# Kernel optimization log

Hardware: AMD Instinct MI355X
Metric: run time of the kernel (lower is better)

## Reference

```python
import jax, jax.numpy as jnp
import numpy as np

N_NODES = 16000
N_EDGES = 128000
IN_FEAT = 1024   # nb_iprs
OUT_FEAT = 1024  # RelGraphConv out / embed_dim
N_RELS = 7
NB_GOS = 4096


def setup_inputs() -> dict:
    key = jax.random.key(0)
    ks = jax.random.split(key, 9)
    feat = jax.random.normal(ks[0], (N_NODES, IN_FEAT), dtype=jnp.float32)
    src = jax.random.randint(ks[1], (N_EDGES,), 0, N_NODES, dtype=jnp.int32)
    dst = jax.random.randint(ks[2], (N_EDGES,), 0, N_NODES, dtype=jnp.int32)
    etypes = jax.random.randint(ks[3], (N_EDGES,), 0, N_RELS, dtype=jnp.int32)
    # RelGraphConv params (regularizer=None): per-relation weight, self-loop weight, bias
    s = 1.0 / np.sqrt(IN_FEAT)
    W_rel = jax.random.uniform(ks[4], (N_RELS, IN_FEAT, OUT_FEAT), dtype=jnp.float32, minval=-s, maxval=s)
    W_loop = jax.random.uniform(ks[5], (IN_FEAT, OUT_FEAT), dtype=jnp.float32, minval=-s, maxval=s)
    bias = jnp.zeros((OUT_FEAT,), dtype=jnp.float32)
    # GO embeddings, init U(-k, k) with k = sqrt(1/embed_dim)
    k = 1.0 / np.sqrt(OUT_FEAT)
    go_embed = jax.random.uniform(ks[6], (NB_GOS, OUT_FEAT), dtype=jnp.float32, minval=-k, maxval=k)
    go_rad = jax.random.uniform(ks[7], (NB_GOS, 1), dtype=jnp.float32, minval=-k, maxval=k)
    return {"feat": feat, "src": src, "dst": dst, "etypes": etypes,
            "W_rel": W_rel, "W_loop": W_loop, "bias": bias,
            "go_embed": go_embed, "go_rad": go_rad}


def reference(feat, src, dst, etypes, W_rel, W_loop, bias, go_embed, go_rad):
    n = feat.shape[0]
    # RelGraphConv (sum aggregation, self-loop, bias, no activation):
    # message on edge e: feat[src[e]] @ W_rel[etypes[e]]; by linearity, first
    # segment-sum source features per (dst, rel), then one batched GEMM.
    x_src = feat[src]                                   # [E, in]
    seg = dst.astype(jnp.int32) * N_RELS + etypes       # combined (dst, rel) id
    agg = jax.ops.segment_sum(x_src, seg, num_segments=n * N_RELS)
    agg = agg.reshape(n, N_RELS, IN_FEAT)               # [N, R, in]
    h = jnp.einsum('nri,rio->no', agg, W_rel) + feat @ W_loop + bias  # [N, out]
    # scoring: sigmoid(x @ E_go^T + |rad|)
    logits = jax.nn.sigmoid(h @ go_embed.T + jnp.abs(go_rad).reshape(1, -1))
    return logits
```

## Files before the change

kernel.cpp:

```cpp
#include <hip/hip_runtime.h>
#include <math.h>

#define N_NODES 16000
#define N_EDGES 128000
#define KDIM 1024
#define N_RELS 7
#define NB_GOS 4096
#define KCAT (KDIM * (N_RELS + 1))
#define MPAD 16128

#define BM 128
#define BN 128
#define BK 32
#define CAP2 (N_EDGES + N_RELS * BM)
#define NTILE_E (CAP2 / BM)

typedef __attribute__((ext_vector_type(8))) short bf16x8;
typedef __attribute__((ext_vector_type(8))) unsigned short u16x8;
typedef __attribute__((ext_vector_type(4))) float f32x4;

__device__ __forceinline__ unsigned short f2bf(float f) {
    union { float f; unsigned int u; } v; v.f = f;
    unsigned int u = v.u + 0x7FFFu + ((v.u >> 16) & 1u);
    return (unsigned short)(u >> 16);
}

__device__ __forceinline__ float bf2f(unsigned short u) {
    union { unsigned int u; float f; } v; v.u = (unsigned int)u << 16;
    return v.f;
}

__device__ __forceinline__ void gload16(const void* g, void* lds) {
    __builtin_amdgcn_global_load_lds(
        (const __attribute__((address_space(1))) unsigned int*)g,
        (__attribute__((address_space(3))) unsigned int*)lds, 16, 0, 0);
}


__global__ __launch_bounds__(256) void conv_bf16(const float* __restrict__ in,
                                                 unsigned short* __restrict__ out, int n8) {
    int i = blockIdx.x * 256 + threadIdx.x;
    if (i >= n8) return;
    const float4* in4 = (const float4*)in;
    float4 x = in4[2 * i], y = in4[2 * i + 1];
    u16x8 o;
    o[0] = f2bf(x.x); o[1] = f2bf(x.y); o[2] = f2bf(x.z); o[3] = f2bf(x.w);
    o[4] = f2bf(y.x); o[5] = f2bf(y.y); o[6] = f2bf(y.z); o[7] = f2bf(y.w);
    *(u16x8*)&out[(size_t)i * 8] = o;
}

__global__ __launch_bounds__(256) void conv_cat(const float* __restrict__ in,
                                                unsigned short* __restrict__ Acat) {
    int i = blockIdx.x * 256 + threadIdx.x;
    if (i >= N_NODES * (KDIM / 8)) return;
    int n = i >> 7, c8 = (i & 127) * 8;
    const float4* in4 = (const float4*)(in + (size_t)n * KDIM + c8);
    float4 x = in4[0], y = in4[1];
    u16x8 o;
    o[0] = f2bf(x.x); o[1] = f2bf(x.y); o[2] = f2bf(x.z); o[3] = f2bf(x.w);
    o[4] = f2bf(y.x); o[5] = f2bf(y.y); o[6] = f2bf(y.z); o[7] = f2bf(y.w);
    *(u16x8*)&Acat[(size_t)n * KCAT + c8] = o;
}

__global__ void transpose_w(const float* __restrict__ Wrel,
                            const float* __restrict__ Wloop,
                            unsigned short* __restrict__ WrelT,
                            unsigned short* __restrict__ WloopT) {
    __shared__ float t[32][33];
    int z = blockIdx.z;
    const float* src = (z < N_RELS) ? Wrel + (size_t)z * KDIM * KDIM : Wloop;
    unsigned short* dst = (z < N_RELS) ? WrelT + (size_t)z * KDIM * KDIM : WloopT;
    int tx = threadIdx.x, ty = threadIdx.y;
    int x = blockIdx.x * 32 + tx;
    int y0 = blockIdx.y * 32;
    #pragma unroll
    for (int j = 0; j < 4; j++)
        t[ty + 8 * j][tx] = src[(size_t)(y0 + ty + 8 * j) * KDIM + x];
    __syncthreads();
    #pragma unroll
    for (int j = 0; j < 4; j++) {
        int n = blockIdx.x * 32 + ty + 8 * j;
        dst[(size_t)n * KDIM + y0 + tx] = f2bf(t[tx][ty + 8 * j]);
    }
}

__global__ void transpose_cat(const float* __restrict__ Wrel,
                              const float* __restrict__ Wloop,
                              unsigned short* __restrict__ BT) {
    __shared__ float t[32][33];
    int z = blockIdx.z;
    const float* src = (z == 0) ? Wloop : Wrel + (size_t)(z - 1) * KDIM * KDIM;
    int tx = threadIdx.x, ty = threadIdx.y;
    int x = blockIdx.x * 32 + tx;
    int y0 = blockIdx.y * 32;
    #pragma unroll
    for (int j = 0; j < 4; j++)
        t[ty + 8 * j][tx] = src[(size_t)(y0 + ty + 8 * j) * KDIM + x];
    __syncthreads();
    #pragma unroll
    for (int j = 0; j < 4; j++) {
        int o = blockIdx.x * 32 + ty + 8 * j;
        BT[(size_t)o * KCAT + z * KDIM + y0 + tx] = f2bf(t[tx][ty + 8 * j]);
    }
}


__global__ void zero_ints(int* p, int n) {
    int i = blockIdx.x * 256 + threadIdx.x;
    if (i < n) p[i] = 0;
}

__global__ void hist_dst(const int* __restrict__ dst, int* cnt) {
    int e = blockIdx.x * 256 + threadIdx.x;
    if (e < N_EDGES) atomicAdd(&cnt[dst[e]], 1);
}

__global__ __launch_bounds__(1024) void scan_offs(const int* __restrict__ cnt,
                                                  int* __restrict__ offs) {
    __shared__ int part[1024];
    int t = threadIdx.x;
    int base = t * 16;
    int local[16];
    int s = 0;
    if (base < N_NODES) {
        #pragma unroll
        for (int j = 0; j < 16; j++) { local[j] = cnt[base + j]; s += local[j]; }
    }
    part[t] = s;
    __syncthreads();
    for (int d = 1; d < 1024; d <<= 1) {
        int v = (t >= d) ? part[t - d] : 0;
        __syncthreads();
        part[t] += v;
        __syncthreads();
    }
    if (base < N_NODES) {
        int ex = (t == 0) ? 0 : part[t - 1];
        #pragma unroll
        for (int j = 0; j < 16; j++) { offs[base + j] = ex; ex += local[j]; }
        if (base + 16 == N_NODES) offs[N_NODES] = ex;
    }
}

__global__ void scatter_dst(const int* __restrict__ src, const int* __restrict__ dst,
                            const int* __restrict__ et, const int* __restrict__ offs,
                            int* cursor, int* __restrict__ se) {
    int e = blockIdx.x * 256 + threadIdx.x;
    if (e < N_EDGES) {
        int d = dst[e];
        int p = atomicAdd(&cursor[d], 1);
        se[offs[d] + p] = (src[e] << 3) | et[e];
    }
}

__global__ __launch_bounds__(256) void aggregate(const int* __restrict__ offs,
                                                 const int* __restrict__ se,
                                                 unsigned short* __restrict__ Acat) {
    int n = blockIdx.x;
    int t = threadIdx.x;
    int e0 = offs[n], e1 = offs[n + 1];
    float4 a0 = {0,0,0,0}, a1 = a0, a2 = a0, a3 = a0, a4 = a0, a5 = a0, a6 = a0;
    for (int i = e0; i < e1; i++) {
        int v = se[i];
        int s = v >> 3, r = v & 7;
        ushort4 q = *(const ushort4*)&Acat[(size_t)s * KCAT + t * 4];
        float4 x = { bf2f(q.x), bf2f(q.y), bf2f(q.z), bf2f(q.w) };
        #define ADD4(a) { a.x += x.x; a.y += x.y; a.z += x.z; a.w += x.w; }
        switch (r) {
            case 0: ADD4(a0) break; case 1: ADD4(a1) break;
            case 2: ADD4(a2) break; case 3: ADD4(a3) break;
            case 4: ADD4(a4) break; case 5: ADD4(a5) break;
            default: ADD4(a6) break;
        }
        #undef ADD4
    }
    unsigned short* row = Acat + (size_t)n * KCAT + KDIM;
    #define ST4(rr, a) { ushort4 o; o.x = f2bf(a.x); o.y = f2bf(a.y); \
                         o.z = f2bf(a.z); o.w = f2bf(a.w); \
                         *(ushort4*)(row + rr * KDIM + t * 4) = o; }
    ST4(0, a0) ST4(1, a1) ST4(2, a2) ST4(3, a3) ST4(4, a4) ST4(5, a5) ST4(6, a6)
    #undef ST4
}


template<int MODE, int KD>
__global__ __launch_bounds__(512, 2) void gemm256(
    const unsigned short* __restrict__ A,
    const unsigned short* __restrict__ BT,
    const float* __restrict__ br,
    void* __restrict__ outv)
{
    __shared__ unsigned short As[2][256 * 64];
    __shared__ unsigned short Bs[2][256 * 64];

    const int tid = threadIdx.x;
    const int l = tid & 63, w = tid >> 6;
    const int wm = w >> 2, wn = w & 3;
    const int lrow = l & 15, lhi = l >> 4, lx = l & 7;

    const int nwg = gridDim.x * gridDim.y;
    const int b = blockIdx.y * gridDim.x + blockIdx.x;
    const int q8 = nwg >> 3, r8 = nwg & 7;
    const int xcd = b & 7, idx = b >> 3;
    const int wg = (xcd < r8 ? xcd * (q8 + 1) : r8 * (q8 + 1) + (xcd - r8) * q8) + idx;
    const int m0 = (wg % gridDim.y) * 256;
    const int n0 = (wg / gridDim.y) * 256;

    const int NI = (KD >> 6) >> 1;

    const int rr = tid >> 3;
    const int cc = (tid & 7) ^ (rr & 7);

    const unsigned short* gA = A + (size_t)(m0 + rr) * KD + cc * 8;
    const unsigned short* gB = BT + (size_t)(n0 + (rr & 31) + (rr >> 5) * 64) * KD + cc * 8;

    auto stageA = [&](int dbuf, int kt, int half) {
        #pragma unroll
        for (int j = 0; j < 2; j++)
            gload16(gA + (size_t)(j * 128 + half * 64) * KD + kt * 64,
                    &As[dbuf][(size_t)(w * 8 + j * 128 + half * 64) * 64]);
    };
    auto stageB = [&](int dbuf, int kt, int half) {
        #pragma unroll
        for (int j = 0; j < 2; j++)
            gload16(gB + (size_t)(j * 128 + half * 32) * KD + kt * 64,
                    &Bs[dbuf][(size_t)((w & 3) * 8 + (w >> 2) * 64 + j * 128 + half * 32) * 64]);
    };

    stageA(0, 0, 0); stageB(0, 0, 0); stageA(0, 0, 1); stageB(0, 0, 1);
    stageA(1, 1, 0); stageB(1, 1, 0);
    asm volatile("s_waitcnt vmcnt(4)" ::: "memory");
    __builtin_amdgcn_s_barrier();

    f32x4 acc[8][4] = {};
    bf16x8 b0[2][2], b1[2][2];

#define LDB(BUF, NH, DST) do { _Pragma("unroll")                              \
    for (int nj = 0; nj < 2; nj++) { _Pragma("unroll")                        \
        for (int ks = 0; ks < 2; ks++) {                                      \
            const int row_ = wn * 64 + (NH) * 32 + nj * 16 + lrow;            \
            const int ch_ = (ks * 4 + lhi) ^ lx;                              \
            DST[nj][ks] = *(const bf16x8*)&Bs[BUF][row_ * 64 + ch_ * 8];      \
        } } } while (0)

#define PH(BUF, MH) do { _Pragma("unroll")                                    \
    for (int mi = 0; mi < 4; mi++) {                                          \
        const int row_ = wm * 128 + (MH) * 64 + mi * 16 + lrow;               \
        bf16x8 a0_ = *(const bf16x8*)&As[BUF][row_ * 64 + (lhi ^ lx) * 8];    \
        bf16x8 a1_ = *(const bf16x8*)&As[BUF][row_ * 64 + ((4 + lhi) ^ lx) * 8];\
        __builtin_amdgcn_s_setprio(1);                                        \
        _Pragma("unroll")                                                     \
        for (int nj = 0; nj < 2; nj++) {                                      \
            acc[(MH)*4+mi][nj] = __builtin_amdgcn_mfma_f32_16x16x32_bf16(     \
                a0_, b0[nj][0], acc[(MH)*4+mi][nj], 0, 0, 0);                 \
            acc[(MH)*4+mi][nj] = __builtin_amdgcn_mfma_f32_16x16x32_bf16(     \
                a1_, b0[nj][1], acc[(MH)*4+mi][nj], 0, 0, 0);                 \
            acc[(MH)*4+mi][2+nj] = __builtin_amdgcn_mfma_f32_16x16x32_bf16(   \
                a0_, b1[nj][0], acc[(MH)*4+mi][2+nj], 0, 0, 0);               \
            acc[(MH)*4+mi][2+nj] = __builtin_amdgcn_mfma_f32_16x16x32_bf16(   \
                a1_, b1[nj][1], acc[(MH)*4+mi][2+nj], 0, 0, 0);               \
        }                                                                     \
        __builtin_amdgcn_s_setprio(0);                                        \
    } } while (0)

    for (int t = 0; t < NI; t++) {
        const bool nl = (t + 1 < NI);
        LDB(0, 0, b0); LDB(0, 1, b1);
        stageA(1, 2 * t + 1, 1); stageB(1, 2 * t + 1, 1);
        PH(0, 0);
        __builtin_amdgcn_s_barrier();
        if (nl) { stageA(0, 2 * t + 2, 0); stageB(0, 2 * t + 2, 0); }
        PH(0, 1);
        if (nl) asm volatile("s_waitcnt vmcnt(4)" ::: "memory");
        else    asm volatile("s_waitcnt vmcnt(0)" ::: "memory");
        __builtin_amdgcn_s_barrier();
        LDB(1, 0, b0); LDB(1, 1, b1);
        if (nl) { stageA(0, 2 * t + 2, 1); stageB(0, 2 * t + 2, 1); }
        PH(1, 0);
        __builtin_amdgcn_s_barrier();
        if (nl) { stageA(1, 2 * t + 3, 0); stageB(1, 2 * t + 3, 0); }
        PH(1, 1);
        if (nl) asm volatile("s_waitcnt vmcnt(4)" ::: "memory");
        else    asm volatile("s_waitcnt vmcnt(0)" ::: "memory");
        __builtin_amdgcn_s_barrier();
    }
#undef LDB
#undef PH

    const int cl = l & 15, rh = (l >> 4) * 4;
    float brv[4];
    #pragma unroll
    for (int nj = 0; nj < 4; nj++) brv[nj] = br[n0 + wn * 64 + nj * 16 + cl];
    #pragma unroll
    for (int mi = 0; mi < 8; mi++) {
        #pragma unroll
        for (int r4 = 0; r4 < 4; r4++) {
            const int row = m0 + wm * 128 + mi * 16 + rh + r4;
            if (MODE == 2 && row >= N_NODES) continue;
            #pragma unroll
            for (int nj = 0; nj < 4; nj++) {
                const int col = n0 + wn * 64 + nj * 16 + cl;
                float x = acc[mi][nj][r4];
                if (MODE == 0) {
                    ((unsigned short*)outv)[(size_t)row * KDIM + col] = f2bf(x + brv[nj]);
                } else {
                    x += fabsf(brv[nj]);
                    ((float*)outv)[(size_t)row * (size_t)NB_GOS + col] =
                        1.0f / (1.0f + __expf(-x));
                }
            }
        }
    }
}


__global__ void init_buckets(int* cnt, int* cursor, int* bucket) {
    int i = blockIdx.x * 256 + threadIdx.x;
    if (i < 8) { cnt[i] = 0; cursor[i] = 0; }
    if (i < CAP2) bucket[i] = -1;
}

__global__ __launch_bounds__(256) void count_etypes(const int* __restrict__ et, int* cnt) {
    __shared__ int lc[N_RELS];
    if (threadIdx.x < N_RELS) lc[threadIdx.x] = 0;
    __syncthreads();
    int e = blockIdx.x * 256 + threadIdx.x;
    if (e < N_EDGES) atomicAdd(&lc[et[e]], 1);
    __syncthreads();
    if (threadIdx.x < N_RELS) atomicAdd(&cnt[threadIdx.x], lc[threadIdx.x]);
}

__global__ void calc_offsets(const int* __restrict__ cnt, int* offs) {
    if (blockIdx.x == 0 && threadIdx.x == 0) {
        int acc = 0;
        offs[0] = 0;
        for (int r = 0; r < N_RELS; r++) {
            acc += ((cnt[r] + BM - 1) / BM) * BM;
            offs[r + 1] = acc;
        }
    }
}

__global__ __launch_bounds__(256) void scatter_edges(const int* __restrict__ et,
                                                     const int* __restrict__ offs,
                                                     int* cursor, int* bucket) {
    __shared__ int lc[N_RELS];
    __shared__ int lbase[N_RELS];
    if (threadIdx.x < N_RELS) lc[threadIdx.x] = 0;
    __syncthreads();
    int e = blockIdx.x * 256 + threadIdx.x;
    int r = 0, my = 0;
    bool valid = (e < N_EDGES);
    if (valid) { r = et[e]; my = atomicAdd(&lc[r], 1); }
    __syncthreads();
    if (threadIdx.x < N_RELS)
        lbase[threadIdx.x] = atomicAdd(&cursor[threadIdx.x], lc[threadIdx.x]);
    __syncthreads();
    if (valid) bucket[offs[r] + lbase[r] + my] = e;
}

template<int MODE>
__global__ __launch_bounds__(256) void mfma_gemm(
    const unsigned short* __restrict__ A,
    const unsigned short* __restrict__ BT,
    const float* __restrict__ br,
    float* __restrict__ out,
    const int* __restrict__ src,
    const int* __restrict__ dst,
    const int* __restrict__ bucket,
    const int* __restrict__ offs,
    int kd)
{
    __shared__ unsigned short As[BM * BK];
    __shared__ unsigned short Bs[BN * BK];
    __shared__ int s_src[BM];
    __shared__ int s_dst[BM];

    const int tid = threadIdx.x;
    const int l = tid & 63;
    const int w = tid >> 6;
    const int wr = w >> 1, wc = w & 1;

    const int nwg = gridDim.x * gridDim.y;
    const int b = blockIdx.y * gridDim.x + blockIdx.x;
    const int cpx = nwg >> 3;
    const int swz = (b & 7) * cpx + (b >> 3);
    const int n0 = (swz / gridDim.y) * BN;
    const int m0 = (swz % gridDim.y) * BM;

    const unsigned short* Bb = BT;
    if (MODE == 1) {
        int rel = -1;
        #pragma unroll
        for (int q = 0; q < N_RELS; q++)
            if (m0 >= offs[q] && m0 < offs[q + 1]) rel = q;
        if (rel < 0) return;
        Bb = BT + (size_t)rel * KDIM * KDIM;
        if (tid < BM) {
            int e = bucket[m0 + tid];
            s_src[tid] = (e >= 0) ? src[e] : -1;
            s_dst[tid] = (e >= 0) ? dst[e] : -1;
        }
        __syncthreads();
    }

    f32x4 acc[4][4] = {};

    const int s0 = tid, s1 = tid + 256;
    const int r0 = s0 >> 2, kc0 = (s0 & 3) * 8;
    const int r1 = s1 >> 2, kc1 = (s1 & 3) * 8;
    unsigned short* ldsA0 = As + (w * 64) * 8;
    unsigned short* ldsA1 = As + (w * 64 + 256) * 8;
    unsigned short* ldsB0 = Bs + (w * 64) * 8;
    unsigned short* ldsB1 = Bs + (w * 64 + 256) * 8;

    size_t arow0, arow1;
    if (MODE == 1) {
        int sr0 = s_src[r0]; arow0 = (sr0 < 0) ? 0 : (size_t)sr0;
        int sr1 = s_src[r1]; arow1 = (sr1 < 0) ? 0 : (size_t)sr1;
    } else {
        arow0 = (size_t)(m0 + r0);
        arow1 = (size_t)(m0 + r1);
    }
    const size_t brow0 = (size_t)(n0 + r0), brow1 = (size_t)(n0 + r1);

    const int fa = (wr * 64 + (l & 15)) * BK + (l >> 4) * 8;
    const int fb = (wc * 64 + (l & 15)) * BK + (l >> 4) * 8;

    for (int k0 = 0; k0 < kd; k0 += BK) {
        gload16(A + arow0 * kd + k0 + kc0, ldsA0);
        gload16(A + arow1 * kd + k0 + kc1, ldsA1);
        gload16(Bb + brow0 * kd + k0 + kc0, ldsB0);
        gload16(Bb + brow1 * kd + k0 + kc1, ldsB1);
        __syncthreads();

        bf16x8 a[4], bfr[4];
        #pragma unroll
        for (int mi = 0; mi < 4; mi++)
            a[mi] = *(const bf16x8*)&As[fa + mi * 16 * BK];
        #pragma unroll
        for (int nj = 0; nj < 4; nj++)
            bfr[nj] = *(const bf16x8*)&Bs[fb + nj * 16 * BK];
        #pragma unroll
        for (int mi = 0; mi < 4; mi++)
            #pragma unroll
            for (int nj = 0; nj < 4; nj++)
                acc[mi][nj] = __builtin_amdgcn_mfma_f32_16x16x32_bf16(a[mi], bfr[nj], acc[mi][nj], 0, 0, 0);
        __syncthreads();
    }

    const int cl = l & 15, rh = (l >> 4) * 4;
    #pragma unroll
    for (int mi = 0; mi < 4; mi++) {
        #pragma unroll
        for (int r4 = 0; r4 < 4; r4++) {
            const int row = wr * 64 + mi * 16 + rh + r4;
            if (MODE == 1) {
                const int d = s_dst[row];
                if (d >= 0) {
                    #pragma unroll
                    for (int nj = 0; nj < 4; nj++) {
                        const int col = n0 + wc * 64 + nj * 16 + cl;
                        atomicAdd(&out[(size_t)d * KDIM + col], acc[mi][nj][r4]);
                    }
                }
            } else if (MODE == 0) {
                #pragma unroll
                for (int nj = 0; nj < 4; nj++) {
                    const int col = n0 + wc * 64 + nj * 16 + cl;
                    out[(size_t)(m0 + row) * KDIM + col] = acc[mi][nj][r4] + br[col];
                }
            } else {
                #pragma unroll
                for (int nj = 0; nj < 4; nj++) {
                    const int col = n0 + wc * 64 + nj * 16 + cl;
                    float x = acc[mi][nj][r4] + fabsf(br[col]);
                    out[(size_t)(m0 + row) * (size_t)NB_GOS + col] = 1.0f / (1.0f + expf(-x));
                }
            }
        }
    }
}


extern "C" void kernel_launch(void* const* d_in, const int* in_sizes, int n_in,
                              void* d_out, int out_size, void* d_ws, size_t ws_size,
                              hipStream_t stream) {
    const float* feat   = (const float*)d_in[0];
    const int*   src    = (const int*)d_in[1];
    const int*   dst    = (const int*)d_in[2];
    const int*   etypes = (const int*)d_in[3];
    const float* W_rel  = (const float*)d_in[4];
    const float* W_loop = (const float*)d_in[5];
    const float* bias   = (const float*)d_in[6];
    const float* go_emb = (const float*)d_in[7];
    const float* go_rad = (const float*)d_in[8];
    float* out = (float*)d_out;

    const size_t ACAT_B = (size_t)MPAD * KCAT * 2;
    const size_t HB_B   = (size_t)MPAD * KDIM * 2;
    const size_t BTC_B  = (size_t)KDIM * KCAT * 2;
    const size_t GOB_B  = (size_t)NB_GOS * KDIM * 2;
    const size_t CNT_B  = 16384 * 4;
    const size_t NEED   = ACAT_B + HB_B + BTC_B + GOB_B + 3 * CNT_B + (size_t)N_EDGES * 4;

    if (ws_size >= NEED) {
        char* p = (char*)d_ws;
        unsigned short* Acat  = (unsigned short*)p;  p += ACAT_B;
        unsigned short* hb    = (unsigned short*)p;  p += HB_B;
        unsigned short* BTcat = (unsigned short*)p;  p += BTC_B;
        unsigned short* gob   = (unsigned short*)p;  p += GOB_B;
        int* cnt    = (int*)p;                       p += CNT_B;
        int* cursor = (int*)p;                       p += CNT_B;
        int* offs   = (int*)p;                       p += CNT_B;
        int* se     = (int*)p;

        zero_ints<<<(2 * 16384 + 255) / 256, 256, 0, stream>>>(cnt, 2 * 16384);
        conv_cat<<<(N_NODES * (KDIM / 8) + 255) / 256, 256, 0, stream>>>(feat, Acat);
        conv_bf16<<<(NB_GOS * KDIM / 8 + 255) / 256, 256, 0, stream>>>(go_emb, gob, NB_GOS * KDIM / 8);
        {
            dim3 g(KDIM / 32, KDIM / 32, N_RELS + 1), bb(32, 8);
            transpose_cat<<<g, bb, 0, stream>>>(W_rel, W_loop, BTcat);
        }
        hist_dst<<<(N_EDGES + 255) / 256, 256, 0, stream>>>(dst, cnt);
        scan_offs<<<1, 1024, 0, stream>>>(cnt, offs);
        scatter_dst<<<(N_EDGES + 255) / 256, 256, 0, stream>>>(src, dst, etypes, offs, cursor, se);
        aggregate<<<N_NODES, 256, 0, stream>>>(offs, se, Acat);

        {
            dim3 g(KDIM / 256, MPAD / 256);
            gemm256<0, KCAT><<<g, 512, 0, stream>>>(Acat, BTcat, bias, hb);
        }
        {
            dim3 g(NB_GOS / 256, MPAD / 256);
            gemm256<2, KDIM><<<g, 512, 0, stream>>>(hb, gob, go_rad, out);
        }
        return;
    }

    char* p = (char*)d_ws;
    float* h            = (float*)p;            p += (size_t)N_NODES * KDIM * 4;
    unsigned short* fb  = (unsigned short*)p;   p += (size_t)N_NODES * KDIM * 2;
    unsigned short* wrT = (unsigned short*)p;   p += (size_t)N_RELS * KDIM * KDIM * 2;
    unsigned short* wlT = (unsigned short*)p;   p += (size_t)KDIM * KDIM * 2;
    unsigned short* gob = (unsigned short*)p;   p += (size_t)NB_GOS * KDIM * 2;
    int* cnt    = (int*)p;
    int* cursor = cnt + 8;
    int* offs   = cursor + 8;
    int* bucket = offs + 16;

    conv_bf16<<<(N_NODES * KDIM / 8 + 255) / 256, 256, 0, stream>>>(feat, fb, N_NODES * KDIM / 8);
    conv_bf16<<<(NB_GOS * KDIM / 8 + 255) / 256, 256, 0, stream>>>(go_emb, gob, NB_GOS * KDIM / 8);
    {
        dim3 g(KDIM / 32, KDIM / 32, N_RELS + 1), bb(32, 8);
        transpose_w<<<g, bb, 0, stream>>>(W_rel, W_loop, wrT, wlT);
    }
    init_buckets<<<(CAP2 + 255) / 256, 256, 0, stream>>>(cnt, cursor, bucket);
    count_etypes<<<(N_EDGES + 255) / 256, 256, 0, stream>>>(etypes, cnt);
    calc_offsets<<<1, 64, 0, stream>>>(cnt, offs);
    scatter_edges<<<(N_EDGES + 255) / 256, 256, 0, stream>>>(etypes, offs, cursor, bucket);
    {
        dim3 g(KDIM / BN, N_NODES / BM);
        mfma_gemm<0><<<g, 256, 0, stream>>>(fb, wlT, bias, h, nullptr, nullptr, nullptr, nullptr, KDIM);
    }
    {
        dim3 g(KDIM / BN, NTILE_E);
        mfma_gemm<1><<<g, 256, 0, stream>>>(fb, wrT, nullptr, h, src, dst, bucket, offs, KDIM);
    }
    conv_bf16<<<(N_NODES * KDIM / 8 + 255) / 256, 256, 0, stream>>>(h, fb, N_NODES * KDIM / 8);
    {
        dim3 g(NB_GOS / BN, N_NODES / BM);
        mfma_gemm<2><<<g, 256, 0, stream>>>(fb, gob, go_rad, out, nullptr, nullptr, nullptr, nullptr, KDIM);
    }
}
```

Measured before the change: 634.7 us.

## Replace 256x256 BK64 GEMM with 128x256 BK32 triple-buffered pipeline

The GEMM kernel moves from a 256x256 output tile with BK=64 double buffering to a 128x256 tile with BK=32 and a three-stage LDS ring, using a new XOR swizzle. This shrinks shared memory and accumulator registers so launch bounds allow four blocks per CU, and it doubles the grid along M. The goal is more occupancy and better hiding of load latency. In exchange, each loaded byte is reused across fewer output elements and there is one barrier per short K step.

```diff
diff --git a/kernel.cpp b/kernel.cpp
--- a/kernel.cpp
+++ b/kernel.cpp
@@ -184,118 +184,89 @@
 
 
 template<int MODE, int KD>
-__global__ __launch_bounds__(512, 2) void gemm256(
+__global__ __launch_bounds__(512, 4) void gemm128(
     const unsigned short* __restrict__ A,
     const unsigned short* __restrict__ BT,
     const float* __restrict__ br,
     void* __restrict__ outv)
 {
-    __shared__ unsigned short As[2][256 * 64];
-    __shared__ unsigned short Bs[2][256 * 64];
+    __shared__ unsigned short As[3][128 * 32];
+    __shared__ unsigned short Bs[3][256 * 32];
 
     const int tid = threadIdx.x;
     const int l = tid & 63, w = tid >> 6;
     const int wm = w >> 2, wn = w & 3;
-    const int lrow = l & 15, lhi = l >> 4, lx = l & 7;
+    const int lrow = l & 15, lhi = l >> 4;
+    const int chl = lhi ^ (lrow & 3) ^ ((lrow >> 2) & 3);
 
     const int nwg = gridDim.x * gridDim.y;
     const int b = blockIdx.y * gridDim.x + blockIdx.x;
     const int q8 = nwg >> 3, r8 = nwg & 7;
     const int xcd = b & 7, idx = b >> 3;
     const int wg = (xcd < r8 ? xcd * (q8 + 1) : r8 * (q8 + 1) + (xcd - r8) * q8) + idx;
-    const int m0 = (wg % gridDim.y) * 256;
+    const int m0 = (wg % gridDim.y) * 128;
     const int n0 = (wg / gridDim.y) * 256;
 
-    const int NI = (KD >> 6) >> 1;
-
-    const int rr = tid >> 3;
-    const int cc = (tid & 7) ^ (rr & 7);
-
-    const unsigned short* gA = A + (size_t)(m0 + rr) * KD + cc * 8;
-    const unsigned short* gB = BT + (size_t)(n0 + (rr & 31) + (rr >> 5) * 64) * KD + cc * 8;
-
-    auto stageA = [&](int dbuf, int kt, int half) {
-        #pragma unroll
-        for (int j = 0; j < 2; j++)
-            gload16(gA + (size_t)(j * 128 + half * 64) * KD + kt * 64,
-                    &As[dbuf][(size_t)(w * 8 + j * 128 + half * 64) * 64]);
+    const int NT = KD >> 5;
+
+    const int rr = tid >> 2;
+    const int cc = (tid & 3) ^ (rr & 3) ^ ((rr >> 2) & 3);
+
+    const unsigned short* gAp = A + (size_t)(m0 + rr) * KD + cc * 8;
+    const unsigned short* gBp = BT + (size_t)(n0 + rr) * KD + cc * 8;
+
+    auto stageA = [&](int dbuf, int kt) {
+        gload16(gAp + kt * 32, &As[dbuf][w * 512]);
     };
-    auto stageB = [&](int dbuf, int kt, int half) {
-        #pragma unroll
-        for (int j = 0; j < 2; j++)
-            gload16(gB + (size_t)(j * 128 + half * 32) * KD + kt * 64,
-                    &Bs[dbuf][(size_t)((w & 3) * 8 + (w >> 2) * 64 + j * 128 + half * 32) * 64]);
+    auto stageB = [&](int dbuf, int kt) {
+        gload16(gBp + kt * 32, &Bs[dbuf][w * 512]);
+        gload16(gBp + (size_t)128 * KD + kt * 32, &Bs[dbuf][4096 + w * 512]);
     };
 
-    stageA(0, 0, 0); stageB(0, 0, 0); stageA(0, 0, 1); stageB(0, 0, 1);
-    stageA(1, 1, 0); stageB(1, 1, 0);
-    asm volatile("s_waitcnt vmcnt(4)" ::: "memory");
+    stageA(0, 0); stageB(0, 0);
+    stageA(1, 1); stageB(1, 1);
+    asm volatile("s_waitcnt vmcnt(3)" ::: "memory");
     __builtin_amdgcn_s_barrier();
 
-    f32x4 acc[8][4] = {};
-    bf16x8 b0[2][2], b1[2][2];
-
-#define LDB(BUF, NH, DST) do { _Pragma("unroll")                              \
-    for (int nj = 0; nj < 2; nj++) { _Pragma("unroll")                        \
-        for (int ks = 0; ks < 2; ks++) {                                      \
-            const int row_ = wn * 64 + (NH) * 32 + nj * 16 + lrow;            \
-            const int ch_ = (ks * 4 + lhi) ^ lx;                              \
-            DST[nj][ks] = *(const bf16x8*)&Bs[BUF][row_ * 64 + ch_ * 8];      \
-        } } } while (0)
-
-#define PH(BUF, MH) do { _Pragma("unroll")                                    \
-    for (int mi = 0; mi < 4; mi++) {                                          \
-        const int row_ = wm * 128 + (MH) * 64 + mi * 16 + lrow;               \
-        bf16x8 a0_ = *(const bf16x8*)&As[BUF][row_ * 64 + (lhi ^ lx) * 8];    \
-        bf16x8 a1_ = *(const bf16x8*)&As[BUF][row_ * 64 + ((4 + lhi) ^ lx) * 8];\
-        __builtin_amdgcn_s_setprio(1);                                        \
-        _Pragma("unroll")                                                     \
-        for (int nj = 0; nj < 2; nj++) {                                      \
-            acc[(MH)*4+mi][nj] = __builtin_amdgcn_mfma_f32_16x16x32_bf16(     \
-                a0_, b0[nj][0], acc[(MH)*4+mi][nj], 0, 0, 0);                 \
-            acc[(MH)*4+mi][nj] = __builtin_amdgcn_mfma_f32_16x16x32_bf16(     \
-                a1_, b0[nj][1], acc[(MH)*4+mi][nj], 0, 0, 0);                 \
-            acc[(MH)*4+mi][2+nj] = __builtin_amdgcn_mfma_f32_16x16x32_bf16(   \
-                a0_, b1[nj][0], acc[(MH)*4+mi][2+nj], 0, 0, 0);               \
-            acc[(MH)*4+mi][2+nj] = __builtin_amdgcn_mfma_f32_16x16x32_bf16(   \
-                a1_, b1[nj][1], acc[(MH)*4+mi][2+nj], 0, 0, 0);               \
-        }                                                                     \
-        __builtin_amdgcn_s_setprio(0);                                        \
-    } } while (0)
-
-    for (int t = 0; t < NI; t++) {
-        const bool nl = (t + 1 < NI);
-        LDB(0, 0, b0); LDB(0, 1, b1);
-        stageA(1, 2 * t + 1, 1); stageB(1, 2 * t + 1, 1);
-        PH(0, 0);
+    f32x4 acc[4][4] = {};
+
+    int cur = 0;
+    for (int kt = 0; kt < NT; kt++) {
+        bf16x8 afr[4], bfr[4];
+        #pragma unroll
+        for (int mi = 0; mi < 4; mi++)
+            afr[mi] = *(const bf16x8*)&As[cur][(wm * 64 + mi * 16 + lrow) * 32 + chl * 8];
+        #pragma unroll
+        for (int nj = 0; nj < 4; nj++)
+            bfr[nj] = *(const bf16x8*)&Bs[cur][(wn * 64 + nj * 16 + lrow) * 32 + chl * 8];
+
+        int st = cur + 2; if (st >= 3) st -= 3;
+        if (kt + 2 < NT) { stageA(st, kt + 2); stageB(st, kt + 2); }
+
+        __builtin_amdgcn_s_setprio(1);
+        #pragma unroll
+        for (int mi = 0; mi < 4; mi++)
+            #pragma unroll
+            for (int nj = 0; nj < 4; nj++)
+                acc[mi][nj] = __builtin_amdgcn_mfma_f32_16x16x32_bf16(
+                    afr[mi], bfr[nj], acc[mi][nj], 0, 0, 0);
+        __builtin_amdgcn_s_setprio(0);
+
+        if (kt + 2 < NT)      asm volatile("s_waitcnt vmcnt(3)" ::: "memory");
+        else if (kt + 1 < NT) asm volatile("s_waitcnt vmcnt(0)" ::: "memory");
         __builtin_amdgcn_s_barrier();
-        if (nl) { stageA(0, 2 * t + 2, 0); stageB(0, 2 * t + 2, 0); }
-        PH(0, 1);
-        if (nl) asm volatile("s_waitcnt vmcnt(4)" ::: "memory");
-        else    asm volatile("s_waitcnt vmcnt(0)" ::: "memory");
-        __builtin_amdgcn_s_barrier();
-        LDB(1, 0, b0); LDB(1, 1, b1);
-        if (nl) { stageA(0, 2 * t + 2, 1); stageB(0, 2 * t + 2, 1); }
-        PH(1, 0);
-        __builtin_amdgcn_s_barrier();
-        if (nl) { stageA(1, 2 * t + 3, 0); stageB(1, 2 * t + 3, 0); }
-        PH(1, 1);
-        if (nl) asm volatile("s_waitcnt vmcnt(4)" ::: "memory");
-        else    asm volatile("s_waitcnt vmcnt(0)" ::: "memory");
-        __builtin_amdgcn_s_barrier();
-    }
-#undef LDB
-#undef PH
+        cur++; if (cur == 3) cur = 0;
+    }
 
     const int cl = l & 15, rh = (l >> 4) * 4;
     float brv[4];
     #pragma unroll
     for (int nj = 0; nj < 4; nj++) brv[nj] = br[n0 + wn * 64 + nj * 16 + cl];
     #pragma unroll
-    for (int mi = 0; mi < 8; mi++) {
+    for (int mi = 0; mi < 4; mi++) {
         #pragma unroll
         for (int r4 = 0; r4 < 4; r4++) {
-            const int row = m0 + wm * 128 + mi * 16 + rh + r4;
+            const int row = m0 + wm * 64 + mi * 16 + rh + r4;
             if (MODE == 2 && row >= N_NODES) continue;
             #pragma unroll
             for (int nj = 0; nj < 4; nj++) {
@@ -528,12 +499,12 @@
         aggregate<<<N_NODES, 256, 0, stream>>>(offs, se, Acat);
 
         {
-            dim3 g(KDIM / 256, MPAD / 256);
-            gemm256<0, KCAT><<<g, 512, 0, stream>>>(Acat, BTcat, bias, hb);
+            dim3 g(KDIM / 256, MPAD / 128);
+            gemm128<0, KCAT><<<g, 512, 0, stream>>>(Acat, BTcat, bias, hb);
         }
         {
-            dim3 g(NB_GOS / 256, MPAD / 256);
-            gemm256<2, KDIM><<<g, 512, 0, stream>>>(hb, gob, go_rad, out);
+            dim3 g(NB_GOS / 256, MPAD / 128);
+            gemm128<2, KDIM><<<g, 512, 0, stream>>>(hb, gob, go_rad, out);
         }
         return;
     }
```

Result: faster. 571.2 us (-10.0%).
